# Kernel tuning notes

Measured on AMD Instinct MI355X. Metric: run time of the kernel, lower is better.

The kernel has to match this reference:

```python
import jax, jax.numpy as jnp
import numpy as np

B, H, L, D = 2, 16, 4096, 128
F_DIM = 64          # feature_dim -> phi dim is 2*F_DIM
S_BLK = 64          # block_size
EPS = 1e-6
SCALING = D ** -0.5


def setup_inputs() -> dict:
    key = jax.random.key(0)
    ks = jax.random.split(key, 4)
    return {
        "query_states": jax.random.normal(ks[0], (B, H, L, D), dtype=jnp.float32),
        "key_states": jax.random.normal(ks[1], (B, H, L, D), dtype=jnp.float32),
        "value_states": jax.random.normal(ks[2], (B, H, L, D), dtype=jnp.float32),
        "hedgehog_weights": jax.random.normal(ks[3], (H, D, F_DIM), dtype=jnp.float32),
        "alpha": jnp.float32(4.0),
    }


def _feature_map(x, weights):
    # x: (B,H,N,S,D) -> (B,H,N,S,2F) = cat(softmax(u), softmax(-u))
    u = jnp.einsum('bhnsd,hdf->bhnsf', x, weights)
    return jnp.concatenate([jax.nn.softmax(u, axis=-1),
                            jax.nn.softmax(-u, axis=-1)], axis=-1)


def reference(query_states, key_states, value_states, hedgehog_weights, alpha):
    b, h, l, d = query_states.shape
    n_blocks = l // S_BLK  # L chosen divisible by block_size (no pad path)

    def to_blocks(x):
        return x.reshape(b, h, n_blocks, S_BLK, d)

    q = to_blocks(query_states)
    k = to_blocks(key_states)
    v = to_blocks(value_states)

    phi_q = _feature_map(q, hedgehog_weights)  # (B,H,N,S,2F)
    phi_k = _feature_map(k, hedgehog_weights)

    w = jax.nn.sigmoid(alpha)

    # scan over blocks; carry the running linear-attention state
    def step(carry, inputs):
        S_state, Z_state = carry            # (B,H,2F,D), (B,H,2F)
        pq, pk, qn, kn, vn = inputs         # each (B,H,S,*)
        denom = jnp.maximum(jnp.einsum('bhsf,bhf->bhs', pq, Z_state), EPS)
        linear_out = jnp.einsum('bhsf,bhfd->bhsd', pq, S_state) / denom[..., None]
        S_state = S_state + jnp.einsum('bhsf,bhsd->bhfd', pk, vn)
        Z_state = Z_state + pk.sum(axis=-2)
        scores = jnp.einsum('bhsd,bhtd->bhst', qn, kn) * SCALING
        softmax_out = jnp.einsum('bhst,bhtd->bhsd', jax.nn.softmax(scores, axis=-1), vn)
        out_n = w * softmax_out + (1.0 - w) * linear_out
        return (S_state, Z_state), out_n

    # move block axis to front for scan: (N,B,H,S,*)
    xs = tuple(jnp.moveaxis(a, 2, 0) for a in (phi_q, phi_k, q, k, v))
    S0 = jnp.zeros((b, h, 2 * F_DIM, d), dtype=jnp.float32)
    Z0 = jnp.zeros((b, h, 2 * F_DIM), dtype=jnp.float32)
    _, out_blocks = jax.lax.scan(step, (S0, Z0), xs)  # (N,B,H,S,D)

    out = jnp.moveaxis(out_blocks, 0, 2).reshape(b, h, l, d)
    return out
```

## Files before the change

### kernel.cpp

```cpp
#include <hip/hip_runtime.h>
#include <math.h>

#define B_ 2
#define H_ 16
#define L_ 4096
#define D_ 128
#define F_ 64
#define F2_ 128
#define S_ 64
#define N_ 64
#define BH_ 32
#define NBT_ 2048
#define EPS_ 1e-6f
#define SCALING_ 0.08838834764831845f

typedef float f32x4 __attribute__((ext_vector_type(4)));
typedef short s16x8 __attribute__((ext_vector_type(8)));
typedef short s16x4 __attribute__((ext_vector_type(4)));

#define MFMA(a, b, c) __builtin_amdgcn_mfma_f32_16x16x32_bf16(a, b, c, 0, 0, 0)


__device__ __forceinline__ short f2bf(float f) {
  unsigned u = __float_as_uint(f);
  u += 0x7fffu + ((u >> 16) & 1u);
  return (short)(u >> 16);
}
__device__ __forceinline__ float bf2f(short s) {
  return __uint_as_float(((unsigned)(unsigned short)s) << 16);
}
__device__ __forceinline__ s16x8 pack8(f32x4 a, f32x4 b) {
  s16x8 r;
  r[0] = f2bf(a[0]); r[1] = f2bf(a[1]); r[2] = f2bf(a[2]); r[3] = f2bf(a[3]);
  r[4] = f2bf(b[0]); r[5] = f2bf(b[1]); r[6] = f2bf(b[2]); r[7] = f2bf(b[3]);
  return r;
}
__device__ __forceinline__ s16x8 frag_f32(const float* p) {
  f32x4 a = *(const f32x4*)p;
  f32x4 b = *(const f32x4*)(p + 4);
  return pack8(a, b);
}

__device__ __forceinline__ s16x8 swz_frag(const short* base, int row, int rowBytes, int colByte) {
  int byte = row * rowBytes + (colByte ^ ((row & 7) << 4));
  return *(const s16x8*)((const char*)base + byte);
}
__device__ __forceinline__ void lds_w16(short* lds, int row, int rowBytes, int colByte, short v) {
  int byte = row * rowBytes + (colByte ^ ((row & 7) << 4));
  *(short*)((char*)lds + byte) = v;
}

__global__ __launch_bounds__(256)
void prep_w(const float* __restrict__ W, short* __restrict__ Wfm)
{
  const int h = blockIdx.x;
  const int tid = threadIdx.x;
  const int f = tid & 63, gq = tid >> 6;
  const float* Wh = W + (size_t)h * D_ * F_;
  short buf[32];
#pragma unroll
  for (int j = 0; j < 32; ++j) buf[j] = f2bf(Wh[(size_t)(gq * 32 + j) * F_ + f]);
  short* Wo = Wfm + (size_t)h * 8192 + ((((f >> 4) * 4 + gq)) << 9);
#pragma unroll
  for (int gp = 0; gp < 4; ++gp) {
    s16x8 v;
#pragma unroll
    for (int e = 0; e < 8; ++e) v[e] = buf[gp * 8 + e];
    *(s16x8*)(Wo + ((gp << 4) + (f & 15)) * 8) = v;
  }
}

__global__ __launch_bounds__(256, 3)
void bslh_phase1(const float* __restrict__ K, const float* __restrict__ V,
                 const short* __restrict__ Wfm, short* __restrict__ Vfm,
                 short* __restrict__ Kfm, short* __restrict__ Sfm,
                 short* __restrict__ dZ)
{
  __shared__ __align__(16) char lds[32 * 1024];
  short* phiT = (short*)lds;
  short* VTs = (short*)(lds + 16384);

  const int blk = blockIdx.x;
  const int bh = blk / N_;
  const int h = bh % H_;
  const int tid = threadIdx.x;
  const int wave = tid >> 6, lane = tid & 63;
  const int rl = lane & 15, g = lane >> 4, kl = g * 8;
  const int r0 = wave * 16;

  const float* Kb = K + (size_t)blk * (S_ * D_);
  const short* Wh = Wfm + (size_t)h * 8192;
  const f32x4 z4 = {0.f, 0.f, 0.f, 0.f};

  f32x4 vv[8];
  {
    const f32x4* gv = (const f32x4*)(V + (size_t)blk * S_ * D_);
#pragma unroll
    for (int ii = 0; ii < 8; ++ii) vv[ii] = gv[tid + 256 * ii];
  }
  f32x4 kv[8];
  {
    const float* kp = Kb + (size_t)(r0 + rl) * D_ + kl;
#pragma unroll
    for (int i = 0; i < 8; ++i) kv[i] = *(const f32x4*)(kp + (i >> 1) * 32 + (i & 1) * 4);
  }

#pragma unroll
  for (int ii = 0; ii < 8; ++ii) {
    int idx = tid + 256 * ii;
    int s = idx >> 5, c = (idx & 31) * 4;
    float m0 = vv[ii][0], m1 = vv[ii][1], m2 = vv[ii][2], m3 = vv[ii][3];
    float o0 = __shfl_xor(m0, 32, 64);
    float o1 = __shfl_xor(m1, 32, 64);
    float o2 = __shfl_xor(m2, 32, 64);
    float o3 = __shfl_xor(m3, 32, 64);
    if (!(tid & 32)) {
      float m[4] = {m0, m1, m2, m3};
      float o[4] = {o0, o1, o2, o3};
#pragma unroll
      for (int j = 0; j < 4; ++j) {
        int d = c + j;
        unsigned pk = (unsigned)(unsigned short)f2bf(m[j]) |
                      ((unsigned)(unsigned short)f2bf(o[j]) << 16);
        int byte = d * 128 + ((s * 2) ^ ((d & 7) << 4));
        *(unsigned*)((char*)VTs + byte) = pk;
      }
    }
  }

  s16x8 aq[4];
#pragma unroll
  for (int ks = 0; ks < 4; ++ks) aq[ks] = pack8(kv[2 * ks], kv[2 * ks + 1]);
  {
    short* Ko = Kfm + (size_t)blk * 8192;
#pragma unroll
    for (int ks = 0; ks < 4; ++ks)
      *(s16x8*)(Ko + (((wave * 4 + ks)) << 9) + lane * 8) = aq[ks];
  }

  f32x4 uacc[4] = {z4, z4, z4, z4};
#pragma unroll
  for (int ks = 0; ks < 4; ++ks) {
#pragma unroll
    for (int tn = 0; tn < 4; ++tn) {
      s16x8 b = *(const s16x8*)(Wh + (((tn * 4 + ks)) << 9) + lane * 8);
      uacc[tn] = MFMA(aq[ks], b, uacc[tn]);
    }
  }

#pragma unroll
  for (int reg = 0; reg < 4; ++reg) {
    float mx = -1e30f, mn = 1e30f;
#pragma unroll
    for (int tn = 0; tn < 4; ++tn) {
      mx = fmaxf(mx, uacc[tn][reg]);
      mn = fminf(mn, uacc[tn][reg]);
    }
#pragma unroll
    for (int o = 1; o <= 8; o <<= 1) {
      mx = fmaxf(mx, __shfl_xor(mx, o, 64));
      mn = fminf(mn, __shfl_xor(mn, o, 64));
    }
    float ep[4], em[4], sp = 0.f, sm = 0.f;
#pragma unroll
    for (int tn = 0; tn < 4; ++tn) {
      ep[tn] = __expf(uacc[tn][reg] - mx); sp += ep[tn];
      em[tn] = __expf(mn - uacc[tn][reg]); sm += em[tn];
    }
#pragma unroll
    for (int o = 1; o <= 8; o <<= 1) {
      sp += __shfl_xor(sp, o, 64);
      sm += __shfl_xor(sm, o, 64);
    }
    const float rp = 1.f / sp, rm = 1.f / sm;
    const int srow = r0 + g * 4 + reg;
#pragma unroll
    for (int tn = 0; tn < 4; ++tn) {
      int f = tn * 16 + rl;
      lds_w16(phiT, f,      2 * S_, srow * 2, f2bf(ep[tn] * rp));
      lds_w16(phiT, f + 64, 2 * S_, srow * 2, f2bf(em[tn] * rm));
    }
  }
  __syncthreads();

  {
    short* Vo = Vfm + (size_t)blk * 8192;
#pragma unroll
    for (int i = 0; i < 4; ++i) {
      int unit = i * 256 + tid;
      int l = unit & 63, ks = (unit >> 6) & 1, tn = unit >> 7;
      int d = tn * 16 + (l & 15);
      int sb = (ks * 32 + (l >> 4) * 8) * 2;
      s16x8 v = *(const s16x8*)((const char*)VTs + d * 128 + (sb ^ ((d & 7) << 4)));
      *(s16x8*)(Vo + unit * 8) = v;
    }
  }

  {
    const int f = tid >> 1, half = tid & 1;
    float z = 0.f;
#pragma unroll
    for (int j2 = 0; j2 < 4; ++j2) {
      s16x8 v = swz_frag(phiT, f, 2 * S_, (half * 32 + j2 * 8) * 2);
#pragma unroll
      for (int e = 0; e < 8; ++e) z += bf2f(v[e]);
    }
    z += __shfl_xor(z, 1, 64);
    if (half == 0) dZ[(size_t)blk * F2_ + f] = f2bf(z);
  }

  f32x4 acc[2][8];
#pragma unroll
  for (int tm = 0; tm < 2; ++tm)
#pragma unroll
    for (int tn = 0; tn < 8; ++tn) acc[tm][tn] = z4;

#pragma unroll
  for (int ks = 0; ks < 2; ++ks) {
    s16x8 a[2];
#pragma unroll
    for (int tm = 0; tm < 2; ++tm)
      a[tm] = swz_frag(VTs, wave * 32 + tm * 16 + rl, 2 * S_, (ks * 32 + kl) * 2);
#pragma unroll
    for (int tn = 0; tn < 8; ++tn) {
      s16x8 b = swz_frag(phiT, tn * 16 + rl, 2 * S_, (ks * 32 + kl) * 2);
#pragma unroll
      for (int tm = 0; tm < 2; ++tm)
        acc[tm][tn] = MFMA(a[tm], b, acc[tm][tn]);
    }
  }
  __syncthreads();

  short* Stb = (short*)lds;
#pragma unroll
  for (int tm = 0; tm < 2; ++tm)
#pragma unroll
    for (int tn = 0; tn < 8; ++tn)
#pragma unroll
      for (int reg = 0; reg < 4; ++reg) {
        float v0 = acc[tm][tn][reg];
        float v1 = __shfl_xor(v0, 1, 64);
        if (!(lane & 1)) {
          int drow = wave * 32 + tm * 16 + g * 4 + reg;
          int fcol = tn * 16 + rl;
          unsigned pk = (unsigned)(unsigned short)f2bf(v0) |
                        ((unsigned)(unsigned short)f2bf(v1) << 16);
          int byte = drow * 256 + ((fcol * 2) ^ ((drow & 7) << 4));
          *(unsigned*)((char*)Stb + byte) = pk;
        }
      }
  __syncthreads();

  {
    short* So = Sfm + (size_t)blk * 16384;
#pragma unroll
    for (int i = 0; i < 8; ++i) {
      int unit = i * 256 + tid;
      int l = unit & 63, ks = (unit >> 6) & 3, tn = unit >> 8;
      int d = tn * 16 + (l & 15);
      int fb = (ks * 32 + (l >> 4) * 8) * 2;
      s16x8 v = *(const s16x8*)((const char*)Stb + d * 256 + (fb ^ ((d & 7) << 4)));
      *(s16x8*)(So + unit * 8) = v;
    }
  }
}

__global__ __launch_bounds__(256)
void bslh_scan(short* __restrict__ St, short* __restrict__ dZ)
{
  const int tid = threadIdx.x;
  if (blockIdx.x < 512) {
    const int idx = blockIdx.x * 256 + tid;
    const int bh = idx >> 12;
    const int rem = idx & 4095;
    short* p = St + (size_t)bh * N_ * (F2_ * D_) + (size_t)rem * 4;
    float run[4] = {0.f, 0.f, 0.f, 0.f};
    for (int n = 0; n < N_; ++n) {
      s16x4 v = *(const s16x4*)p;
      s16x4 o;
#pragma unroll
      for (int e = 0; e < 4; ++e) {
        o[e] = f2bf(run[e]);
        run[e] += bf2f(v[e]);
      }
      *(s16x4*)p = o;
      p += F2_ * D_;
    }
  } else {
    const int idx = (blockIdx.x - 512) * 256 + tid;
    const int bh = idx >> 5, e = idx & 31;
    short* p = dZ + (size_t)bh * N_ * F2_ + (size_t)e * 4;
    float run[4] = {0.f, 0.f, 0.f, 0.f};
    for (int n = 0; n < N_; ++n) {
      s16x4 v = *(const s16x4*)p;
      s16x4 o;
#pragma unroll
      for (int e2 = 0; e2 < 4; ++e2) {
        o[e2] = f2bf(run[e2]);
        run[e2] += bf2f(v[e2]);
      }
      *(s16x4*)p = o;
      p += F2_;
    }
  }
}

__global__ __launch_bounds__(256, 4)
void bslh_phase3(const float* __restrict__ Q, const short* __restrict__ Kfm,
                 const short* __restrict__ Vfm, const short* __restrict__ Wfm,
                 const short* __restrict__ Sfm, const short* __restrict__ Zp,
                 const float* __restrict__ alphap, float* __restrict__ Out)
{
  __shared__ __align__(16) short phi[S_ * F2_];
  __shared__ __align__(16) short Pl[S_ * S_];
  __shared__ float clL[S_];

  const int blk = blockIdx.x;
  const int bh = blk / N_;
  const int h = bh % H_;
  const int tid = threadIdx.x;
  const int wave = tid >> 6, lane = tid & 63;
  const int rl = lane & 15, g = lane >> 4, kl = g * 8;
  const int r0 = wave * 16;

  const float* Qb = Q + (size_t)blk * (S_ * D_);
  const short* Kb = Kfm + (size_t)blk * 8192;
  const short* Vb = Vfm + (size_t)blk * 8192;
  const short* Sb = Sfm + (size_t)blk * 16384;
  const short* Wh = Wfm + (size_t)h * 8192;
  const short* Zb = Zp + (size_t)blk * F2_;
  const float w = 1.f / (1.f + __expf(-alphap[0]));
  const f32x4 z4 = {0.f, 0.f, 0.f, 0.f};

  s16x8 aq[4];
  f32x4 uacc[4] = {z4, z4, z4, z4};
  for (int ks = 0; ks < 4; ++ks) {
    aq[ks] = frag_f32(Qb + (size_t)(r0 + rl) * D_ + ks * 32 + kl);
#pragma unroll
    for (int tn = 0; tn < 4; ++tn) {
      s16x8 b = *(const s16x8*)(Wh + (((tn * 4 + ks)) << 9) + lane * 8);
      uacc[tn] = MFMA(aq[ks], b, uacc[tn]);
    }
  }

#pragma unroll
  for (int reg = 0; reg < 4; ++reg) {
    float mx = -1e30f, mn = 1e30f;
#pragma unroll
    for (int tn = 0; tn < 4; ++tn) {
      mx = fmaxf(mx, uacc[tn][reg]);
      mn = fminf(mn, uacc[tn][reg]);
    }
#pragma unroll
    for (int o = 1; o <= 8; o <<= 1) {
      mx = fmaxf(mx, __shfl_xor(mx, o, 64));
      mn = fminf(mn, __shfl_xor(mn, o, 64));
    }
    float ep[4], em[4], sp = 0.f, sm = 0.f;
#pragma unroll
    for (int tn = 0; tn < 4; ++tn) {
      ep[tn] = __expf(uacc[tn][reg] - mx); sp += ep[tn];
      em[tn] = __expf(mn - uacc[tn][reg]); sm += em[tn];
    }
#pragma unroll
    for (int o = 1; o <= 8; o <<= 1) {
      sp += __shfl_xor(sp, o, 64);
      sm += __shfl_xor(sm, o, 64);
    }
    const float rp = 1.f / sp, rm = 1.f / sm;
    const int srow = r0 + g * 4 + reg;
#pragma unroll
    for (int tn = 0; tn < 4; ++tn) {
      int f = tn * 16 + rl;
      lds_w16(phi, srow, 2 * F2_, f * 2,        f2bf(ep[tn] * rp));
      lds_w16(phi, srow, 2 * F2_, (f + 64) * 2, f2bf(em[tn] * rm));
    }
  }
  __syncthreads();

  if (tid < 64) {
    float den = 0.f;
#pragma unroll
    for (int j2 = 0; j2 < 16; ++j2) {
      s16x8 v = swz_frag(phi, tid, 2 * F2_, j2 * 16);
      s16x8 zv = *(const s16x8*)(Zb + j2 * 8);
#pragma unroll
      for (int e = 0; e < 8; ++e) den += bf2f(v[e]) * bf2f(zv[e]);
    }
    clL[tid] = (1.f - w) / fmaxf(den, EPS_);
  }

  f32x4 sacc[4] = {z4, z4, z4, z4};
  for (int ks = 0; ks < 4; ++ks) {
#pragma unroll
    for (int tn = 0; tn < 4; ++tn) {
      s16x8 b = *(const s16x8*)(Kb + (((tn * 4 + ks)) << 9) + lane * 8);
      sacc[tn] = MFMA(aq[ks], b, sacc[tn]);
    }
  }
#pragma unroll
  for (int reg = 0; reg < 4; ++reg) {
    float mx = -1e30f;
#pragma unroll
    for (int tn = 0; tn < 4; ++tn) {
      sacc[tn][reg] *= SCALING_;
      mx = fmaxf(mx, sacc[tn][reg]);
    }
#pragma unroll
    for (int o = 1; o <= 8; o <<= 1) mx = fmaxf(mx, __shfl_xor(mx, o, 64));
    float e_[4], sum = 0.f;
#pragma unroll
    for (int tn = 0; tn < 4; ++tn) {
      e_[tn] = __expf(sacc[tn][reg] - mx);
      sum += e_[tn];
    }
#pragma unroll
    for (int o = 1; o <= 8; o <<= 1) sum += __shfl_xor(sum, o, 64);
    const float pw = w / sum;
    const int srow = r0 + g * 4 + reg;
#pragma unroll
    for (int tn = 0; tn < 4; ++tn)
      lds_w16(Pl, srow, 2 * S_, (tn * 16 + rl) * 2, f2bf(e_[tn] * pw));
  }
  __syncthreads();

  f32x4 acc[8];
#pragma unroll
  for (int tn = 0; tn < 8; ++tn) acc[tn] = z4;

  for (int ks = 0; ks < 4; ++ks) {
    s16x8 a = swz_frag(phi, r0 + rl, 2 * F2_, (ks * 32 + kl) * 2);
#pragma unroll
    for (int tn = 0; tn < 8; ++tn) {
      s16x8 b = *(const s16x8*)(Sb + (((tn * 4 + ks)) << 9) + lane * 8);
      acc[tn] = MFMA(a, b, acc[tn]);
    }
  }
  float cl[4];
#pragma unroll
  for (int reg = 0; reg < 4; ++reg) cl[reg] = clL[r0 + g * 4 + reg];
#pragma unroll
  for (int tn = 0; tn < 8; ++tn)
#pragma unroll
    for (int reg = 0; reg < 4; ++reg) acc[tn][reg] *= cl[reg];

  for (int ks = 0; ks < 2; ++ks) {
    s16x8 a = swz_frag(Pl, r0 + rl, 2 * S_, (ks * 32 + kl) * 2);
#pragma unroll
    for (int tn = 0; tn < 8; ++tn) {
      s16x8 b = *(const s16x8*)(Vb + (((tn * 2 + ks)) << 9) + lane * 8);
      acc[tn] = MFMA(a, b, acc[tn]);
    }
  }

  float* Ob = Out + (size_t)blk * (S_ * D_);
#pragma unroll
  for (int tn = 0; tn < 8; ++tn)
#pragma unroll
    for (int reg = 0; reg < 4; ++reg) {
      int srow = r0 + g * 4 + reg;
      Ob[(size_t)srow * D_ + tn * 16 + rl] = acc[tn][reg];
    }
}

extern "C" void kernel_launch(void* const* d_in, const int* in_sizes, int n_in,
                              void* d_out, int out_size, void* d_ws, size_t ws_size,
                              hipStream_t stream)
{
  const float* Q = (const float*)d_in[0];
  const float* K = (const float*)d_in[1];
  const float* V = (const float*)d_in[2];
  const float* W = (const float*)d_in[3];
  const float* alpha = (const float*)d_in[4];
  float* Out = (float*)d_out;

  short* Vfm = (short*)d_ws;
  short* Sfm = Vfm + (size_t)NBT_ * 8192;
  short* Kfm = Sfm + (size_t)NBT_ * 16384;
  short* dZ = Kfm + (size_t)NBT_ * 8192;
  short* Wfm = dZ + (size_t)NBT_ * F2_;

  hipLaunchKernelGGL(prep_w, dim3(H_), dim3(256), 0, stream, W, Wfm);
  hipLaunchKernelGGL(bslh_phase1, dim3(NBT_), dim3(256), 0, stream,
                     K, V, Wfm, Vfm, Kfm, Sfm, dZ);
  hipLaunchKernelGGL(bslh_scan, dim3(516), dim3(256), 0, stream, Sfm, dZ);
  hipLaunchKernelGGL(bslh_phase3, dim3(NBT_), dim3(256), 0, stream,
                     Q, Kfm, Vfm, Wfm, Sfm, dZ, alpha, Out);
}
```

Measured before the change: 139.5 us.

## Use native bf16 conversions, reswizzle V tile, fuse Vfm store into MFMA loads

Replaces the manual round-to-nearest bf16 conversion with the compiler's __bf16 cast so it can emit packed conversion instructions. The V^T LDS swizzle gains an extra XOR term to reduce bank conflicts on the transposed writes. The separate pass that copied V fragments from LDS to global memory is removed; the fragments already loaded as MFMA A-operands are stored directly. Occupancy hint rises from 3 to 4 blocks per SM, which may force register spills.

```diff
diff --git a/kernel.cpp b/kernel.cpp
--- a/kernel.cpp
+++ b/kernel.cpp
@@ -22,18 +22,24 @@
 
 
 __device__ __forceinline__ short f2bf(float f) {
-  unsigned u = __float_as_uint(f);
-  u += 0x7fffu + ((u >> 16) & 1u);
-  return (short)(u >> 16);
+  __bf16 h = (__bf16)f;
+  return __builtin_bit_cast(short, h);
 }
 __device__ __forceinline__ float bf2f(short s) {
   return __uint_as_float(((unsigned)(unsigned short)s) << 16);
 }
+__device__ __forceinline__ unsigned cvtpk2(float lo, float hi) {
+  unsigned short a = __builtin_bit_cast(unsigned short, (__bf16)lo);
+  unsigned short b = __builtin_bit_cast(unsigned short, (__bf16)hi);
+  return (unsigned)a | ((unsigned)b << 16);
+}
 __device__ __forceinline__ s16x8 pack8(f32x4 a, f32x4 b) {
-  s16x8 r;
-  r[0] = f2bf(a[0]); r[1] = f2bf(a[1]); r[2] = f2bf(a[2]); r[3] = f2bf(a[3]);
-  r[4] = f2bf(b[0]); r[5] = f2bf(b[1]); r[6] = f2bf(b[2]); r[7] = f2bf(b[3]);
-  return r;
+  union { unsigned u[4]; s16x8 s; } r;
+  r.u[0] = cvtpk2(a[0], a[1]);
+  r.u[1] = cvtpk2(a[2], a[3]);
+  r.u[2] = cvtpk2(b[0], b[1]);
+  r.u[3] = cvtpk2(b[2], b[3]);
+  return r.s;
 }
 __device__ __forceinline__ s16x8 frag_f32(const float* p) {
   f32x4 a = *(const f32x4*)p;
@@ -48,6 +54,10 @@
 __device__ __forceinline__ void lds_w16(short* lds, int row, int rowBytes, int colByte, short v) {
   int byte = row * rowBytes + (colByte ^ ((row & 7) << 4));
   *(short*)((char*)lds + byte) = v;
+}
+
+__device__ __forceinline__ int vswz(int d, int colByte) {
+  return d * 128 + (colByte ^ (((d ^ (d >> 2)) & 7) << 4));
 }
 
 __global__ __launch_bounds__(256)
@@ -70,7 +80,7 @@
   }
 }
 
-__global__ __launch_bounds__(256, 3)
+__global__ __launch_bounds__(256, 4)
 void bslh_phase1(const float* __restrict__ K, const float* __restrict__ V,
                  const short* __restrict__ Wfm, short* __restrict__ Vfm,
                  short* __restrict__ Kfm, short* __restrict__ Sfm,
@@ -120,10 +130,8 @@
 #pragma unroll
       for (int j = 0; j < 4; ++j) {
         int d = c + j;
-        unsigned pk = (unsigned)(unsigned short)f2bf(m[j]) |
-                      ((unsigned)(unsigned short)f2bf(o[j]) << 16);
-        int byte = d * 128 + ((s * 2) ^ ((d & 7) << 4));
-        *(unsigned*)((char*)VTs + byte) = pk;
+        unsigned pk = cvtpk2(m[j], o[j]);
+        *(unsigned*)((char*)VTs + vswz(d, s * 2)) = pk;
       }
     }
   }
@@ -184,19 +192,6 @@
   __syncthreads();
 
   {
-    short* Vo = Vfm + (size_t)blk * 8192;
-#pragma unroll
-    for (int i = 0; i < 4; ++i) {
-      int unit = i * 256 + tid;
-      int l = unit & 63, ks = (unit >> 6) & 1, tn = unit >> 7;
-      int d = tn * 16 + (l & 15);
-      int sb = (ks * 32 + (l >> 4) * 8) * 2;
-      s16x8 v = *(const s16x8*)((const char*)VTs + d * 128 + (sb ^ ((d & 7) << 4)));
-      *(s16x8*)(Vo + unit * 8) = v;
-    }
-  }
-
-  {
     const int f = tid >> 1, half = tid & 1;
     float z = 0.f;
 #pragma unroll
@@ -215,18 +210,24 @@
 #pragma unroll
     for (int tn = 0; tn < 8; ++tn) acc[tm][tn] = z4;
 
-#pragma unroll
-  for (int ks = 0; ks < 2; ++ks) {
-    s16x8 a[2];
-#pragma unroll
-    for (int tm = 0; tm < 2; ++tm)
-      a[tm] = swz_frag(VTs, wave * 32 + tm * 16 + rl, 2 * S_, (ks * 32 + kl) * 2);
-#pragma unroll
-    for (int tn = 0; tn < 8; ++tn) {
-      s16x8 b = swz_frag(phiT, tn * 16 + rl, 2 * S_, (ks * 32 + kl) * 2);
-#pragma unroll
-      for (int tm = 0; tm < 2; ++tm)
-        acc[tm][tn] = MFMA(a[tm], b, acc[tm][tn]);
+  {
+    short* Vo = Vfm + (size_t)blk * 8192;
+#pragma unroll
+    for (int ks = 0; ks < 2; ++ks) {
+      s16x8 a[2];
+#pragma unroll
+      for (int tm = 0; tm < 2; ++tm) {
+        int d = wave * 32 + tm * 16 + rl;
+        a[tm] = *(const s16x8*)((const char*)VTs + vswz(d, (ks * 32 + kl) * 2));
+        *(s16x8*)(Vo + ((((2 * wave + tm) * 2 + ks)) << 9) + lane * 8) = a[tm];
+      }
+#pragma unroll
+      for (int tn = 0; tn < 8; ++tn) {
+        s16x8 b = swz_frag(phiT, tn * 16 + rl, 2 * S_, (ks * 32 + kl) * 2);
+#pragma unroll
+        for (int tm = 0; tm < 2; ++tm)
+          acc[tm][tn] = MFMA(a[tm], b, acc[tm][tn]);
+      }
     }
   }
   __syncthreads();
@@ -243,8 +244,7 @@
         if (!(lane & 1)) {
           int drow = wave * 32 + tm * 16 + g * 4 + reg;
           int fcol = tn * 16 + rl;
-          unsigned pk = (unsigned)(unsigned short)f2bf(v0) |
-                        ((unsigned)(unsigned short)f2bf(v1) << 16);
+          unsigned pk = cvtpk2(v0, v1);
           int byte = drow * 256 + ((fcol * 2) ^ ((drow & 7) << 4));
           *(unsigned*)((char*)Stb + byte) = pk;
         }
```

After: 139.3 us. No clear change (-0.1%).
